# Kernel optimization log

Hardware: AMD Instinct MI355X
Metric: run time of the kernel (lower is better)

The kernel has to match this reference:

```python
import jax, jax.numpy as jnp
import numpy as np

INPUT_SIZE = 256
HIDDEN_SIZE = 256


def setup_inputs() -> dict:
    key = jax.random.key(0)
    k_x, k_wxh, k_whh = jax.random.split(key, 3)
    x = jax.random.normal(k_x, (64, 2048, INPUT_SIZE), dtype=jnp.float32)
    # torch nn.Linear weights: [out_features, in_features]
    W_xh = jax.random.normal(k_wxh, (HIDDEN_SIZE, INPUT_SIZE), dtype=jnp.float32) / np.sqrt(INPUT_SIZE)
    W_hh = jax.random.normal(k_whh, (HIDDEN_SIZE, HIDDEN_SIZE), dtype=jnp.float32) / np.sqrt(HIDDEN_SIZE)
    b_h = jnp.zeros((HIDDEN_SIZE,), dtype=jnp.float32)
    return {"x": x, "W_xh": W_xh, "W_hh": W_hh, "b_h": b_h}


def reference(x, W_xh, W_hh, b_h):
    # x: [B, T, D]; h_t = relu(x_t @ W_xh^T + h_{t-1} @ W_hh^T + b_h)
    B, T, _ = x.shape
    # Precompute input projection for all timesteps in one GEMM (same math).
    xproj = jnp.einsum('btd,hd->bth', x, W_xh) + b_h  # [B, T, H]

    def step(h, xp_t):
        h_new = jax.nn.relu(xp_t + h @ W_hh.T)
        return h_new, h_new

    h0 = jnp.zeros((B, HIDDEN_SIZE), dtype=x.dtype)
    # scan over time axis: move T to leading dim
    _, hs = jax.lax.scan(step, h0, jnp.swapaxes(xproj, 0, 1))  # hs: [T, B, H]
    return jnp.swapaxes(hs, 0, 1)  # [B, T, H]
```

## Files before the change

### kernel.cpp

```cpp
#include <hip/hip_runtime.h>

#define BATCH 64
#define SEQT  2048
#define DIM   256
#define HID   256

typedef _Float16 half_t;
typedef _Float16 half2_t __attribute__((ext_vector_type(2)));
typedef _Float16 half4_t __attribute__((ext_vector_type(4)));
typedef _Float16 half8_t __attribute__((ext_vector_type(8)));
typedef float    float4_t __attribute__((ext_vector_type(4)));

__device__ __forceinline__ half8_t cvt8(float4_t a, float4_t b) {
  half8_t r;
  r[0] = (half_t)a[0]; r[1] = (half_t)a[1]; r[2] = (half_t)a[2]; r[3] = (half_t)a[3];
  r[4] = (half_t)b[0]; r[5] = (half_t)b[1]; r[6] = (half_t)b[2]; r[7] = (half_t)b[3];
  return r;
}
#define H2X(v, c) __builtin_shufflevector((v), (v), 2*(c), 2*(c)+1)

template<int CTRL>
__device__ __forceinline__ float dpp_mov(float a) {
  int t = __builtin_amdgcn_mov_dpp(__builtin_bit_cast(int, a), CTRL, 0xF, 0xF, true);
  return __builtin_bit_cast(float, t);
}

__global__ __launch_bounds__(256) void cvt_w_kernel(
    const float* __restrict__ W, half_t* __restrict__ Wh)
{
  const int i = (blockIdx.x * 256 + threadIdx.x) * 4;
  float4_t v = *(const float4_t*)(W + i);
  half4_t o; o[0]=(half_t)v[0]; o[1]=(half_t)v[1]; o[2]=(half_t)v[2]; o[3]=(half_t)v[3];
  *(half4_t*)(Wh + i) = o;
}

__global__ __launch_bounds__(256) void xproj_f16_kernel(
    const float* __restrict__ x, const half_t* __restrict__ Wh,
    const float* __restrict__ bh, float* __restrict__ out)
{
  const int lane = threadIdx.x & 63;
  const int wave = threadIdx.x >> 6;
  const int r16  = lane & 15;
  const int kg   = lane >> 4;
  const long m0  = (long)blockIdx.x * 64 + wave * 16;

  half8_t a[8];
  const float* xr = x + (m0 + r16) * (long)DIM + kg * 8;
  #pragma unroll
  for (int kf = 0; kf < 8; ++kf) {
    float4_t x0 = *(const float4_t*)(xr + kf * 32);
    float4_t x1 = *(const float4_t*)(xr + kf * 32 + 4);
    a[kf] = cvt8(x0, x1);
  }

  #pragma unroll 2
  for (int nt = 0; nt < 16; ++nt) {
    const half_t* wr = Wh + (nt * 16 + r16) * (long)DIM + kg * 8;
    float bb = bh[nt * 16 + r16];
    float4_t acc = {bb, bb, bb, bb};
    #pragma unroll
    for (int kf = 0; kf < 8; ++kf) {
      half8_t bfrag = *(const half8_t*)(wr + kf * 32);
      acc = __builtin_amdgcn_mfma_f32_16x16x32_f16(a[kf], bfrag, acc, 0, 0, 0);
    }
    float* op = out + (m0 + kg * 4) * (long)HID + nt * 16 + r16;
    #pragma unroll
    for (int r = 0; r < 4; ++r) op[(long)r * HID] = acc[r];
  }
}

__global__ __launch_bounds__(256) void xproj_kernel(
    const float* __restrict__ x, const float* __restrict__ Wxh,
    const float* __restrict__ bh, float* __restrict__ out)
{
  const int lane = threadIdx.x & 63;
  const int wave = threadIdx.x >> 6;
  const int r16  = lane & 15;
  const int kg   = lane >> 4;
  const long m0  = (long)blockIdx.x * 64 + wave * 16;

  half8_t a[8];
  const float* xr = x + (m0 + r16) * (long)DIM + kg * 8;
  #pragma unroll
  for (int kf = 0; kf < 8; ++kf) {
    float4_t x0 = *(const float4_t*)(xr + kf * 32);
    float4_t x1 = *(const float4_t*)(xr + kf * 32 + 4);
    a[kf] = cvt8(x0, x1);
  }
  for (int nt = 0; nt < 16; ++nt) {
    const float* wr = Wxh + (nt * 16 + r16) * (long)DIM + kg * 8;
    float bb = bh[nt * 16 + r16];
    float4_t acc = {bb, bb, bb, bb};
    #pragma unroll
    for (int kf = 0; kf < 8; ++kf) {
      float4_t w0 = *(const float4_t*)(wr + kf * 32);
      float4_t w1 = *(const float4_t*)(wr + kf * 32 + 4);
      acc = __builtin_amdgcn_mfma_f32_16x16x32_f16(a[kf], cvt8(w0, w1), acc, 0, 0, 0);
    }
    float* op = out + (m0 + kg * 4) * (long)HID + nt * 16 + r16;
    #pragma unroll
    for (int r = 0; r < 4; ++r) op[(long)r * HID] = acc[r];
  }
}

#define RNN_BAR() asm volatile("s_waitcnt lgkmcnt(0)\n\ts_barrier" ::: "memory")

#define RNN_STEP(U, XQ)                                                        \
  {                                                                            \
    const int t = t4 + (U);                                                    \
         \
    const int tp = (t + 4 < T) ? (t + 4) : (T - 1);                            \
    float xnew = outp[(long)tp * HID];                                         \
    half8_t hv[4];                                                             \
    _Pragma("unroll")                                                          \
    for (int s = 0; s < 4; ++s)                                                \
      hv[s] = *(const half8_t*)(hraw[(U) & 1] + rb + 16 * s);                  \
    float a0 = 0.f, a1 = 0.f, a2 = 0.f, a3 = 0.f;                              \
    _Pragma("unroll")                                                          \
    for (int s = 0; s < 4; ++s) {                                              \
      a0 = __builtin_amdgcn_fdot2(H2X(w8[0][s], 0), H2X(hv[s], 0), a0, false); \
      a0 = __builtin_amdgcn_fdot2(H2X(w8[0][s], 1), H2X(hv[s], 1), a0, false); \
      a0 = __builtin_amdgcn_fdot2(H2X(w8[0][s], 2), H2X(hv[s], 2), a0, false); \
      a0 = __builtin_amdgcn_fdot2(H2X(w8[0][s], 3), H2X(hv[s], 3), a0, false); \
      a1 = __builtin_amdgcn_fdot2(H2X(w8[1][s], 0), H2X(hv[s], 0), a1, false); \
      a1 = __builtin_amdgcn_fdot2(H2X(w8[1][s], 1), H2X(hv[s], 1), a1, false); \
      a1 = __builtin_amdgcn_fdot2(H2X(w8[1][s], 2), H2X(hv[s], 2), a1, false); \
      a1 = __builtin_amdgcn_fdot2(H2X(w8[1][s], 3), H2X(hv[s], 3), a1, false); \
      a2 = __builtin_amdgcn_fdot2(H2X(w8[2][s], 0), H2X(hv[s], 0), a2, false); \
      a2 = __builtin_amdgcn_fdot2(H2X(w8[2][s], 1), H2X(hv[s], 1), a2, false); \
      a2 = __builtin_amdgcn_fdot2(H2X(w8[2][s], 2), H2X(hv[s], 2), a2, false); \
      a2 = __builtin_amdgcn_fdot2(H2X(w8[2][s], 3), H2X(hv[s], 3), a2, false); \
      a3 = __builtin_amdgcn_fdot2(H2X(w8[3][s], 0), H2X(hv[s], 0), a3, false); \
      a3 = __builtin_amdgcn_fdot2(H2X(w8[3][s], 1), H2X(hv[s], 1), a3, false); \
      a3 = __builtin_amdgcn_fdot2(H2X(w8[3][s], 2), H2X(hv[s], 2), a3, false); \
      a3 = __builtin_amdgcn_fdot2(H2X(w8[3][s], 3), H2X(hv[s], 3), a3, false); \
    }                                                                          \
        \
    float r0 = kA ? a0 : a2;                 \
    float r1 = kA ? a1 : a3;                                                   \
    float b0 = (kA ? a2 : a0) + dpp_mov<0x141>(r0);                            \
    float b1 = (kA ? a3 : a1) + dpp_mov<0x141>(r1);                            \
    float rB = kB ? b0 : b1;                 \
    float c  = (kB ? b1 : b0) + dpp_mov<0x4E>(rB);                             \
    float fin = c + dpp_mov<0xB1>(c);            \
    float y = fmaxf(fin + (XQ), 0.f);                                          \
    outp[(long)t * HID] = y;                                                   \
    *(half_t*)(hraw[((U) & 1) ^ 1] + hwb) = (half_t)y;                         \
    XQ = xnew;                                                                 \
    RNN_BAR();                                                                 \
  }

__global__ __launch_bounds__(512, 1) void rnn_kernel(
    const float* __restrict__ Whh, float* __restrict__ out, int T)
{
  __shared__ alignas(128) unsigned char hraw[2][8 * 80];

  const int tid = threadIdx.x;
  const int l   = tid & 63;
  const int w   = tid >> 6;
  const int g   = l & 7;
  const int j0  = w * 32 + (l >> 3) * 4;
  const int rb  = g * 80;
  const int jown = j0 + ((l >> 1) & 3);
  const int hwb = ((jown >> 5) * 80 + (jown & 31) * 2);
  const bool kA = (l & 4) != 0;
  const bool kB = (l & 2) != 0;
  float* outp = out + (long)blockIdx.x * SEQT * HID + jown;

  half8_t w8[4][4];
  #pragma unroll
  for (int i = 0; i < 4; ++i) {
    const float* wr = Whh + (long)(j0 + i) * HID + g * 32;
    #pragma unroll
    for (int s = 0; s < 4; ++s) {
      float4_t v0 = *(const float4_t*)(wr + s * 8);
      float4_t v1 = *(const float4_t*)(wr + s * 8 + 4);
      w8[i][s] = cvt8(v0, v1);
    }
  }

  if (tid < 160) ((float*)hraw[0])[tid] = 0.f;

  float xq0 = outp[0L * HID];
  float xq1 = outp[1L * HID];
  float xq2 = outp[2L * HID];
  float xq3 = outp[3L * HID];
  RNN_BAR();

  #pragma unroll 1
  for (int t4 = 0; t4 < T; t4 += 4) {
    RNN_STEP(0, xq0)
    RNN_STEP(1, xq1)
    RNN_STEP(2, xq2)
    RNN_STEP(3, xq3)
  }
}

extern "C" void kernel_launch(void* const* d_in, const int* in_sizes, int n_in,
                              void* d_out, int out_size, void* d_ws, size_t ws_size,
                              hipStream_t stream) {
  const float* x   = (const float*)d_in[0];
  const float* Wxh = (const float*)d_in[1];
  const float* Whh = (const float*)d_in[2];
  const float* bh  = (const float*)d_in[3];
  float* out = (float*)d_out;

  if (ws_size >= (size_t)(DIM * HID * sizeof(half_t))) {
    half_t* Wh = (half_t*)d_ws;
    cvt_w_kernel<<<dim3((DIM * HID) / 1024), dim3(256), 0, stream>>>(Wxh, Wh);
    xproj_f16_kernel<<<dim3((BATCH * SEQT) / 64), dim3(256), 0, stream>>>(x, Wh, bh, out);
  } else {
    xproj_kernel<<<dim3((BATCH * SEQT) / 64), dim3(256), 0, stream>>>(x, Wxh, bh, out);
  }
  rnn_kernel<<<dim3(BATCH), dim3(512), 0, stream>>>(Whh, out, SEQT);
}
```

Before: 989.7 us.

## Keep Wxh fragments in registers for xproj and regroup RNN dot lanes

The input-projection kernel now loads each wave's slice of the fp16 weight once into registers. It loops over 8 row tiles of 16 per block, so each block covers 128 rows and the grid is halved, instead of re-reading all 16 weight column tiles per 16-row tile. The recurrent kernel changes the work split: each lane now holds 8 output rows times 16 k-elements instead of 4 rows times 32. That halves the LDS h-vector reads per step and widens the DPP reduction tree to 16 lanes with one extra stage. The h buffer layout changes from 80-byte to 48-byte rows to match.

Result: slower. 1.094 ms (+10.6%).

```diff
diff --git a/kernel.cpp b/kernel.cpp
--- a/kernel.cpp
+++ b/kernel.cpp
@@ -34,8 +34,54 @@
   *(half4_t*)(Wh + i) = o;
 }
 
-__global__ __launch_bounds__(256) void xproj_f16_kernel(
+__global__ __launch_bounds__(256) void xproj_f16_v2(
     const float* __restrict__ x, const half_t* __restrict__ Wh,
+    const float* __restrict__ bh, float* __restrict__ out)
+{
+  const int lane = threadIdx.x & 63;
+  const int wave = threadIdx.x >> 6;
+  const int r16  = lane & 15;
+  const int kg   = lane >> 4;
+  const long m0  = (long)blockIdx.x * 128;
+
+  half8_t bfr[4][8];
+  float bb[4];
+  #pragma unroll
+  for (int q = 0; q < 4; ++q) {
+    const int nt = wave * 4 + q;
+    const half_t* wr = Wh + (nt * 16 + r16) * (long)DIM + kg * 8;
+    #pragma unroll
+    for (int kf = 0; kf < 8; ++kf)
+      bfr[q][kf] = *(const half8_t*)(wr + kf * 32);
+    bb[q] = bh[nt * 16 + r16];
+  }
+
+  #pragma unroll 1
+  for (int mi = 0; mi < 8; ++mi) {
+    const long mrow = m0 + mi * 16;
+    half8_t a[8];
+    const float* xr = x + (mrow + r16) * (long)DIM + kg * 8;
+    #pragma unroll
+    for (int kf = 0; kf < 8; ++kf) {
+      float4_t x0 = *(const float4_t*)(xr + kf * 32);
+      float4_t x1 = *(const float4_t*)(xr + kf * 32 + 4);
+      a[kf] = cvt8(x0, x1);
+    }
+    #pragma unroll
+    for (int q = 0; q < 4; ++q) {
+      float4_t acc = {bb[q], bb[q], bb[q], bb[q]};
+      #pragma unroll
+      for (int kf = 0; kf < 8; ++kf)
+        acc = __builtin_amdgcn_mfma_f32_16x16x32_f16(a[kf], bfr[q][kf], acc, 0, 0, 0);
+      float* op = out + (mrow + kg * 4) * (long)HID + (wave * 4 + q) * 16 + r16;
+      #pragma unroll
+      for (int r = 0; r < 4; ++r) op[(long)r * HID] = acc[r];
+    }
+  }
+}
+
+__global__ __launch_bounds__(256) void xproj_kernel(
+    const float* __restrict__ x, const float* __restrict__ Wxh,
     const float* __restrict__ bh, float* __restrict__ out)
 {
   const int lane = threadIdx.x & 63;
@@ -52,41 +98,6 @@
     float4_t x1 = *(const float4_t*)(xr + kf * 32 + 4);
     a[kf] = cvt8(x0, x1);
   }
-
-  #pragma unroll 2
-  for (int nt = 0; nt < 16; ++nt) {
-    const half_t* wr = Wh + (nt * 16 + r16) * (long)DIM + kg * 8;
-    float bb = bh[nt * 16 + r16];
-    float4_t acc = {bb, bb, bb, bb};
-    #pragma unroll
-    for (int kf = 0; kf < 8; ++kf) {
-      half8_t bfrag = *(const half8_t*)(wr + kf * 32);
-      acc = __builtin_amdgcn_mfma_f32_16x16x32_f16(a[kf], bfrag, acc, 0, 0, 0);
-    }
-    float* op = out + (m0 + kg * 4) * (long)HID + nt * 16 + r16;
-    #pragma unroll
-    for (int r = 0; r < 4; ++r) op[(long)r * HID] = acc[r];
-  }
-}
-
-__global__ __launch_bounds__(256) void xproj_kernel(
-    const float* __restrict__ x, const float* __restrict__ Wxh,
-    const float* __restrict__ bh, float* __restrict__ out)
-{
-  const int lane = threadIdx.x & 63;
-  const int wave = threadIdx.x >> 6;
-  const int r16  = lane & 15;
-  const int kg   = lane >> 4;
-  const long m0  = (long)blockIdx.x * 64 + wave * 16;
-
-  half8_t a[8];
-  const float* xr = x + (m0 + r16) * (long)DIM + kg * 8;
-  #pragma unroll
-  for (int kf = 0; kf < 8; ++kf) {
-    float4_t x0 = *(const float4_t*)(xr + kf * 32);
-    float4_t x1 = *(const float4_t*)(xr + kf * 32 + 4);
-    a[kf] = cvt8(x0, x1);
-  }
   for (int nt = 0; nt < 16; ++nt) {
     const float* wr = Wxh + (nt * 16 + r16) * (long)DIM + kg * 8;
     float bb = bh[nt * 16 + r16];
@@ -105,44 +116,49 @@
 
 #define RNN_BAR() asm volatile("s_waitcnt lgkmcnt(0)\n\ts_barrier" ::: "memory")
 
+#define RNN_DOTC(c)                                                            \
+    a0 = __builtin_amdgcn_fdot2(H2X(w8[0][0], c), H2X(hv0, c), a0, false);     \
+    a1 = __builtin_amdgcn_fdot2(H2X(w8[1][0], c), H2X(hv0, c), a1, false);     \
+    a2 = __builtin_amdgcn_fdot2(H2X(w8[2][0], c), H2X(hv0, c), a2, false);     \
+    a3 = __builtin_amdgcn_fdot2(H2X(w8[3][0], c), H2X(hv0, c), a3, false);     \
+    a4 = __builtin_amdgcn_fdot2(H2X(w8[4][0], c), H2X(hv0, c), a4, false);     \
+    a5 = __builtin_amdgcn_fdot2(H2X(w8[5][0], c), H2X(hv0, c), a5, false);     \
+    a6 = __builtin_amdgcn_fdot2(H2X(w8[6][0], c), H2X(hv0, c), a6, false);     \
+    a7 = __builtin_amdgcn_fdot2(H2X(w8[7][0], c), H2X(hv0, c), a7, false);     \
+    a0 = __builtin_amdgcn_fdot2(H2X(w8[0][1], c), H2X(hv1, c), a0, false);     \
+    a1 = __builtin_amdgcn_fdot2(H2X(w8[1][1], c), H2X(hv1, c), a1, false);     \
+    a2 = __builtin_amdgcn_fdot2(H2X(w8[2][1], c), H2X(hv1, c), a2, false);     \
+    a3 = __builtin_amdgcn_fdot2(H2X(w8[3][1], c), H2X(hv1, c), a3, false);     \
+    a4 = __builtin_amdgcn_fdot2(H2X(w8[4][1], c), H2X(hv1, c), a4, false);     \
+    a5 = __builtin_amdgcn_fdot2(H2X(w8[5][1], c), H2X(hv1, c), a5, false);     \
+    a6 = __builtin_amdgcn_fdot2(H2X(w8[6][1], c), H2X(hv1, c), a6, false);     \
+    a7 = __builtin_amdgcn_fdot2(H2X(w8[7][1], c), H2X(hv1, c), a7, false);
+
 #define RNN_STEP(U, XQ)                                                        \
   {                                                                            \
     const int t = t4 + (U);                                                    \
-         \
     const int tp = (t + 4 < T) ? (t + 4) : (T - 1);                            \
     float xnew = outp[(long)tp * HID];                                         \
-    half8_t hv[4];                                                             \
-    _Pragma("unroll")                                                          \
-    for (int s = 0; s < 4; ++s)                                                \
-      hv[s] = *(const half8_t*)(hraw[(U) & 1] + rb + 16 * s);                  \
-    float a0 = 0.f, a1 = 0.f, a2 = 0.f, a3 = 0.f;                              \
-    _Pragma("unroll")                                                          \
-    for (int s = 0; s < 4; ++s) {                                              \
-      a0 = __builtin_amdgcn_fdot2(H2X(w8[0][s], 0), H2X(hv[s], 0), a0, false); \
-      a0 = __builtin_amdgcn_fdot2(H2X(w8[0][s], 1), H2X(hv[s], 1), a0, false); \
-      a0 = __builtin_amdgcn_fdot2(H2X(w8[0][s], 2), H2X(hv[s], 2), a0, false); \
-      a0 = __builtin_amdgcn_fdot2(H2X(w8[0][s], 3), H2X(hv[s], 3), a0, false); \
-      a1 = __builtin_amdgcn_fdot2(H2X(w8[1][s], 0), H2X(hv[s], 0), a1, false); \
-      a1 = __builtin_amdgcn_fdot2(H2X(w8[1][s], 1), H2X(hv[s], 1), a1, false); \
-      a1 = __builtin_amdgcn_fdot2(H2X(w8[1][s], 2), H2X(hv[s], 2), a1, false); \
-      a1 = __builtin_amdgcn_fdot2(H2X(w8[1][s], 3), H2X(hv[s], 3), a1, false); \
-      a2 = __builtin_amdgcn_fdot2(H2X(w8[2][s], 0), H2X(hv[s], 0), a2, false); \
-      a2 = __builtin_amdgcn_fdot2(H2X(w8[2][s], 1), H2X(hv[s], 1), a2, false); \
-      a2 = __builtin_amdgcn_fdot2(H2X(w8[2][s], 2), H2X(hv[s], 2), a2, false); \
-      a2 = __builtin_amdgcn_fdot2(H2X(w8[2][s], 3), H2X(hv[s], 3), a2, false); \
-      a3 = __builtin_amdgcn_fdot2(H2X(w8[3][s], 0), H2X(hv[s], 0), a3, false); \
-      a3 = __builtin_amdgcn_fdot2(H2X(w8[3][s], 1), H2X(hv[s], 1), a3, false); \
-      a3 = __builtin_amdgcn_fdot2(H2X(w8[3][s], 2), H2X(hv[s], 2), a3, false); \
-      a3 = __builtin_amdgcn_fdot2(H2X(w8[3][s], 3), H2X(hv[s], 3), a3, false); \
-    }                                                                          \
-        \
-    float r0 = kA ? a0 : a2;                 \
-    float r1 = kA ? a1 : a3;                                                   \
-    float b0 = (kA ? a2 : a0) + dpp_mov<0x141>(r0);                            \
-    float b1 = (kA ? a3 : a1) + dpp_mov<0x141>(r1);                            \
-    float rB = kB ? b0 : b1;                 \
-    float c  = (kB ? b1 : b0) + dpp_mov<0x4E>(rB);                             \
-    float fin = c + dpp_mov<0xB1>(c);            \
+    half8_t hv0 = *(const half8_t*)(hraw[(U) & 1] + rb);                       \
+    half8_t hv1 = *(const half8_t*)(hraw[(U) & 1] + rb + 16);                  \
+    float a0=0.f,a1=0.f,a2=0.f,a3=0.f,a4=0.f,a5=0.f,a6=0.f,a7=0.f;             \
+    RNN_DOTC(0) RNN_DOTC(1) RNN_DOTC(2) RNN_DOTC(3)                            \
+                                      \
+    float rA0 = s8 ? a0 : a4, rA1 = s8 ? a1 : a5;                              \
+    float rA2 = s8 ? a2 : a6, rA3 = s8 ? a3 : a7;                              \
+    float b0 = (s8 ? a4 : a0) + dpp_mov<0x140>(rA0);                           \
+    float b1 = (s8 ? a5 : a1) + dpp_mov<0x140>(rA1);                           \
+    float b2 = (s8 ? a6 : a2) + dpp_mov<0x140>(rA2);                           \
+    float b3 = (s8 ? a7 : a3) + dpp_mov<0x140>(rA3);                           \
+                                       \
+    float rB0 = s4 ? b0 : b2, rB1 = s4 ? b1 : b3;                              \
+    float c0 = (s4 ? b2 : b0) + dpp_mov<0x141>(rB0);                           \
+    float c1 = (s4 ? b3 : b1) + dpp_mov<0x141>(rB1);                           \
+                                       \
+    float rC = s2 ? c0 : c1;                                                   \
+    float dd = (s2 ? c1 : c0) + dpp_mov<0x4E>(rC);                             \
+                                                 \
+    float fin = dd + dpp_mov<0xB1>(dd);                                        \
     float y = fmaxf(fin + (XQ), 0.f);                                          \
     outp[(long)t * HID] = y;                                                   \
     *(half_t*)(hraw[((U) & 1) ^ 1] + hwb) = (half_t)y;                         \
@@ -153,33 +169,35 @@
 __global__ __launch_bounds__(512, 1) void rnn_kernel(
     const float* __restrict__ Whh, float* __restrict__ out, int T)
 {
-  __shared__ alignas(128) unsigned char hraw[2][8 * 80];
+  __shared__ alignas(128) unsigned char hraw[2][16 * 48];
 
   const int tid = threadIdx.x;
   const int l   = tid & 63;
   const int w   = tid >> 6;
-  const int g   = l & 7;
-  const int j0  = w * 32 + (l >> 3) * 4;
-  const int rb  = g * 80;
-  const int jown = j0 + ((l >> 1) & 3);
-  const int hwb = ((jown >> 5) * 80 + (jown & 31) * 2);
-  const bool kA = (l & 4) != 0;
-  const bool kB = (l & 2) != 0;
+  const int g   = l & 15;
+  const int o   = w * 4 + (l >> 4);
+  const int j0  = o * 8;
+  const int rb  = g * 48;
+  const int jown = j0 + ((l >> 1) & 7);
+  const int hwb = ((jown >> 4) * 48 + (jown & 15) * 2);
+  const bool s8 = (l & 8) != 0;
+  const bool s4 = (l & 4) != 0;
+  const bool s2 = (l & 2) != 0;
   float* outp = out + (long)blockIdx.x * SEQT * HID + jown;
 
-  half8_t w8[4][4];
+  half8_t w8[8][2];
   #pragma unroll
-  for (int i = 0; i < 4; ++i) {
-    const float* wr = Whh + (long)(j0 + i) * HID + g * 32;
-    #pragma unroll
-    for (int s = 0; s < 4; ++s) {
+  for (int i = 0; i < 8; ++i) {
+    const float* wr = Whh + (long)(j0 + i) * HID + g * 16;
+    #pragma unroll
+    for (int s = 0; s < 2; ++s) {
       float4_t v0 = *(const float4_t*)(wr + s * 8);
       float4_t v1 = *(const float4_t*)(wr + s * 8 + 4);
       w8[i][s] = cvt8(v0, v1);
     }
   }
 
-  if (tid < 160) ((float*)hraw[0])[tid] = 0.f;
+  if (tid < 192) ((float*)hraw[0])[tid] = 0.f;
 
   float xq0 = outp[0L * HID];
   float xq1 = outp[1L * HID];
@@ -208,7 +226,7 @@
   if (ws_size >= (size_t)(DIM * HID * sizeof(half_t))) {
     half_t* Wh = (half_t*)d_ws;
     cvt_w_kernel<<<dim3((DIM * HID) / 1024), dim3(256), 0, stream>>>(Wxh, Wh);
-    xproj_f16_kernel<<<dim3((BATCH * SEQT) / 64), dim3(256), 0, stream>>>(x, Wh, bh, out);
+    xproj_f16_v2<<<dim3((BATCH * SEQT) / 128), dim3(256), 0, stream>>>(x, Wh, bh, out);
   } else {
     xproj_kernel<<<dim3((BATCH * SEQT) / 64), dim3(256), 0, stream>>>(x, Wxh, bh, out);
   }
```

## Keep W_xh fragments register-resident and loop over row tiles in xproj

Applied to the files above, without the earlier changes.

Rewrites the input-projection GEMM so each wave preloads its 64-column slice of the half-precision weight matrix into registers once. It then iterates over 8 row tiles of x, with each block covering 128 rows. This removes repeated weight fetches per 16-row tile, at the cost of each wave reloading and converting the same x rows, and higher register use. The RNN recurrence kernel is unchanged.

Measured after the change: 940.7 us. 1.05x faster.

```diff
diff --git a/kernel.cpp b/kernel.cpp
--- a/kernel.cpp
+++ b/kernel.cpp
@@ -25,6 +25,8 @@
   return __builtin_bit_cast(float, t);
 }
 
+#define RNN_BAR() asm volatile("s_waitcnt lgkmcnt(0)\n\ts_barrier" ::: "memory")
+
 __global__ __launch_bounds__(256) void cvt_w_kernel(
     const float* __restrict__ W, half_t* __restrict__ Wh)
 {
@@ -34,8 +36,53 @@
   *(half4_t*)(Wh + i) = o;
 }
 
-__global__ __launch_bounds__(256) void xproj_f16_kernel(
+__global__ __launch_bounds__(256) void xproj_f16_v2(
     const float* __restrict__ x, const half_t* __restrict__ Wh,
+    const float* __restrict__ bh, float* __restrict__ out)
+{
+  const int lane = threadIdx.x & 63;
+  const int wave = threadIdx.x >> 6;
+  const int r16  = lane & 15;
+  const int kg   = lane >> 4;
+  const long m0  = (long)blockIdx.x * 128;
+
+  half8_t bfr[4][8];
+  float bb[4];
+  #pragma unroll
+  for (int qq = 0; qq < 4; ++qq) {
+    const int nt = wave * 4 + qq;
+    const half_t* wr = Wh + (nt * 16 + r16) * (long)DIM + kg * 8;
+    #pragma unroll
+    for (int kf = 0; kf < 8; ++kf)
+      bfr[qq][kf] = *(const half8_t*)(wr + kf * 32);
+    bb[qq] = bh[nt * 16 + r16];
+  }
+  #pragma unroll 1
+  for (int mi = 0; mi < 8; ++mi) {
+    const long mrow = m0 + mi * 16;
+    half8_t a[8];
+    const float* xr = x + (mrow + r16) * (long)DIM + kg * 8;
+    #pragma unroll
+    for (int kf = 0; kf < 8; ++kf) {
+      float4_t x0 = *(const float4_t*)(xr + kf * 32);
+      float4_t x1 = *(const float4_t*)(xr + kf * 32 + 4);
+      a[kf] = cvt8(x0, x1);
+    }
+    #pragma unroll
+    for (int qq = 0; qq < 4; ++qq) {
+      float4_t acc = {bb[qq], bb[qq], bb[qq], bb[qq]};
+      #pragma unroll
+      for (int kf = 0; kf < 8; ++kf)
+        acc = __builtin_amdgcn_mfma_f32_16x16x32_f16(a[kf], bfr[qq][kf], acc, 0, 0, 0);
+      float* op = out + (mrow + kg * 4) * (long)HID + (wave * 4 + qq) * 16 + r16;
+      #pragma unroll
+      for (int r = 0; r < 4; ++r) op[(long)r * HID] = acc[r];
+    }
+  }
+}
+
+__global__ __launch_bounds__(256) void xproj_kernel(
+    const float* __restrict__ x, const float* __restrict__ Wxh,
     const float* __restrict__ bh, float* __restrict__ out)
 {
   const int lane = threadIdx.x & 63;
@@ -52,41 +99,6 @@
     float4_t x1 = *(const float4_t*)(xr + kf * 32 + 4);
     a[kf] = cvt8(x0, x1);
   }
-
-  #pragma unroll 2
-  for (int nt = 0; nt < 16; ++nt) {
-    const half_t* wr = Wh + (nt * 16 + r16) * (long)DIM + kg * 8;
-    float bb = bh[nt * 16 + r16];
-    float4_t acc = {bb, bb, bb, bb};
-    #pragma unroll
-    for (int kf = 0; kf < 8; ++kf) {
-      half8_t bfrag = *(const half8_t*)(wr + kf * 32);
-      acc = __builtin_amdgcn_mfma_f32_16x16x32_f16(a[kf], bfrag, acc, 0, 0, 0);
-    }
-    float* op = out + (m0 + kg * 4) * (long)HID + nt * 16 + r16;
-    #pragma unroll
-    for (int r = 0; r < 4; ++r) op[(long)r * HID] = acc[r];
-  }
-}
-
-__global__ __launch_bounds__(256) void xproj_kernel(
-    const float* __restrict__ x, const float* __restrict__ Wxh,
-    const float* __restrict__ bh, float* __restrict__ out)
-{
-  const int lane = threadIdx.x & 63;
-  const int wave = threadIdx.x >> 6;
-  const int r16  = lane & 15;
-  const int kg   = lane >> 4;
-  const long m0  = (long)blockIdx.x * 64 + wave * 16;
-
-  half8_t a[8];
-  const float* xr = x + (m0 + r16) * (long)DIM + kg * 8;
-  #pragma unroll
-  for (int kf = 0; kf < 8; ++kf) {
-    float4_t x0 = *(const float4_t*)(xr + kf * 32);
-    float4_t x1 = *(const float4_t*)(xr + kf * 32 + 4);
-    a[kf] = cvt8(x0, x1);
-  }
   for (int nt = 0; nt < 16; ++nt) {
     const float* wr = Wxh + (nt * 16 + r16) * (long)DIM + kg * 8;
     float bb = bh[nt * 16 + r16];
@@ -103,12 +115,9 @@
   }
 }
 
-#define RNN_BAR() asm volatile("s_waitcnt lgkmcnt(0)\n\ts_barrier" ::: "memory")
-
 #define RNN_STEP(U, XQ)                                                        \
   {                                                                            \
     const int t = t4 + (U);                                                    \
-         \
     const int tp = (t + 4 < T) ? (t + 4) : (T - 1);                            \
     float xnew = outp[(long)tp * HID];                                         \
     half8_t hv[4];                                                             \
@@ -208,7 +217,7 @@
   if (ws_size >= (size_t)(DIM * HID * sizeof(half_t))) {
     half_t* Wh = (half_t*)d_ws;
     cvt_w_kernel<<<dim3((DIM * HID) / 1024), dim3(256), 0, stream>>>(Wxh, Wh);
-    xproj_f16_kernel<<<dim3((BATCH * SEQT) / 64), dim3(256), 0, stream>>>(x, Wh, bh, out);
+    xproj_f16_v2<<<dim3((BATCH * SEQT) / 128), dim3(256), 0, stream>>>(x, Wh, bh, out);
   } else {
     xproj_kernel<<<dim3((BATCH * SEQT) / 64), dim3(256), 0, stream>>>(x, Wxh, bh, out);
   }
```
